# Kernel tuning notes

Measured on AMD Instinct MI355X. Metric: run time of the kernel, lower is better.

The kernel has to match this reference:

```python
import jax, jax.numpy as jnp
import numpy as np

B = 8388608  # batch rows
D = 4        # n_inputs
N_EPH = 2


def setup_inputs() -> dict:
    key = jax.random.key(0)
    kx, ke = jax.random.split(key)
    X = jax.random.normal(kx, (B, D), dtype=jnp.float32)
    ephs = jax.random.uniform(ke, (N_EPH,), dtype=jnp.float32)
    return {"X": X, "ephs": ephs}


def reference(X, ephs):
    # Fixed active CGP DAG (matches a concrete genome of CGPModel):
    # inputs x0..x3, ephemeral constants c0, c1.
    # Interior function nodes are pure elementwise ops evaluated in
    # topological order along the active paths, outputs stacked on dim=1.
    x0, x1, x2, x3 = X[:, 0], X[:, 1], X[:, 2], X[:, 3]
    c0, c1 = ephs[0], ephs[1]
    n4 = x0 * x1                 # mul(x0, x1)
    n5 = jnp.sin(n4 + c0)        # sin(add(n4, c0))
    n6 = x2 * x3                 # mul(x2, x3)
    n7 = n5 * n6 + jnp.sin(x2)   # add(mul(n5, n6), sin(x2))
    n8 = jnp.cos(n7) * c1 + x0   # add(mul(cos(n7), c1), x0)
    # two output nodes -> stack to (B, 2)
    return jnp.stack([n7, n8], axis=1)
```

## Files before the change

kernel.cpp:

```cpp
#include <hip/hip_runtime.h>
#include <hip/hip_bf16.h>


__global__ __launch_bounds__(256) void cgp_kernel(const float4* __restrict__ X,
                                                  const float* __restrict__ ephs,
                                                  float2* __restrict__ out,
                                                  int B) {
    int i = blockIdx.x * blockDim.x + threadIdx.x;
    if (i >= B) return;

    const float c0 = ephs[0];
    const float c1 = ephs[1];

    float4 x = X[i];

    float n4 = x.x * x.y;
    float n5 = __sinf(0.0f);
    n5 = sinf(n4 + c0);
    float n6 = x.z * x.w;
    float n7 = fmaf(n5, n6, sinf(x.z));
    float n8 = fmaf(cosf(n7), c1, x.x);

    out[i] = make_float2(n7, n8);
}

extern "C" void kernel_launch(void* const* d_in, const int* in_sizes, int n_in,
                              void* d_out, int out_size, void* d_ws, size_t ws_size,
                              hipStream_t stream) {
    const float4* X  = (const float4*)d_in[0];
    const float* eph = (const float*)d_in[1];
    float2* out      = (float2*)d_out;
    int B = in_sizes[0] / 4;

    int block = 256;
    int grid = (B + block - 1) / block;
    cgp_kernel<<<grid, block, 0, stream>>>(X, eph, out, B);
}
```

Baseline: 202.4 us.

## Use fast sin/cos intrinsics and grid-stride loop with 4-way unrolled rows

Replaces the accurate sinf/cosf calls with the hardware __sinf/__cosf intrinsics to cut the transcendental cost per row. It also changes the launch to a fixed 2048-block grid-stride loop that loads four rows per iteration, giving more memory-level parallelism. The intrinsics have lower accuracy, especially for large arguments, which may affect tolerance checks.

```diff
diff --git a/kernel.cpp b/kernel.cpp
--- a/kernel.cpp
+++ b/kernel.cpp
@@ -1,27 +1,45 @@
 #include <hip/hip_runtime.h>
-#include <hip/hip_bf16.h>
 
+
+__device__ __forceinline__ float2 cgp_row(float4 x, float c0, float c1) {
+    float n4 = x.x * x.y;
+    float n5 = __sinf(n4 + c0);
+    float n6 = x.z * x.w;
+    float n7 = fmaf(n5, n6, __sinf(x.z));
+    float n8 = fmaf(__cosf(n7), c1, x.x);
+    return make_float2(n7, n8);
+}
 
 __global__ __launch_bounds__(256) void cgp_kernel(const float4* __restrict__ X,
                                                   const float* __restrict__ ephs,
                                                   float2* __restrict__ out,
                                                   int B) {
-    int i = blockIdx.x * blockDim.x + threadIdx.x;
-    if (i >= B) return;
-
     const float c0 = ephs[0];
     const float c1 = ephs[1];
 
-    float4 x = X[i];
+    const int tid = blockIdx.x * blockDim.x + threadIdx.x;
+    const int T   = gridDim.x * blockDim.x;
 
-    float n4 = x.x * x.y;
-    float n5 = __sinf(0.0f);
-    n5 = sinf(n4 + c0);
-    float n6 = x.z * x.w;
-    float n7 = fmaf(n5, n6, sinf(x.z));
-    float n8 = fmaf(cosf(n7), c1, x.x);
+    int base = tid;
+    for (; base + 3 * T < B; base += 4 * T) {
+        float4 a = X[base];
+        float4 b = X[base + T];
+        float4 c = X[base + 2 * T];
+        float4 d = X[base + 3 * T];
 
-    out[i] = make_float2(n7, n8);
+        float2 ra = cgp_row(a, c0, c1);
+        float2 rb = cgp_row(b, c0, c1);
+        float2 rc = cgp_row(c, c0, c1);
+        float2 rd = cgp_row(d, c0, c1);
+
+        out[base]         = ra;
+        out[base + T]     = rb;
+        out[base + 2 * T] = rc;
+        out[base + 3 * T] = rd;
+    }
+    for (; base < B; base += T) {
+        out[base] = cgp_row(X[base], c0, c1);
+    }
 }
 
 extern "C" void kernel_launch(void* const* d_in, const int* in_sizes, int n_in,
@@ -32,7 +50,7 @@
     float2* out      = (float2*)d_out;
     int B = in_sizes[0] / 4;
 
-    int block = 256;
-    int grid = (B + block - 1) / block;
+    const int block = 256;
+    const int grid  = 2048;
     cgp_kernel<<<grid, block, 0, stream>>>(X, eph, out, B);
 }
```

Result: slower. 214.9 us (+6.2%).
